# Performance work log

Measured on AMD Instinct MI355X. Metric: run time of the kernel, lower is better.

Reference implementation:

```python
import jax, jax.numpy as jnp
import numpy as np

LN_EPS = 1e-5

def _moe_forward(x, Wg, bg, W1, b1, W2, b2, ln_w, ln_b, gate_scale, top_k=2):
    B, N, D = x.shape
    E = Wg.shape[1]
    x_flat = x.reshape(B * N, D)                      # [T, D]
    # --- router (MoEGate): softmax -> top-k -> renormalize ---
    logits = x_flat @ Wg + bg                         # [T, E]
    probs = jax.nn.softmax(logits, axis=-1)
    w, idx = jax.lax.top_k(probs, top_k)              # [T, k]
    w = w / jnp.sum(w, axis=-1, keepdims=True)
    # dense gate matrix [T, E]: scatter top-k weights onto their experts
    gates = jnp.sum(jax.nn.one_hot(idx, E, dtype=x.dtype) * w[..., None], axis=1)
    # --- experts: Linear -> GELU(erf) -> Linear, computed densely for all experts ---
    h = jax.nn.gelu(jnp.einsum('td,edo->eto', x_flat, W1) + b1[:, None, :],
                    approximate=False)                # [E, T, O]
    eo = jnp.einsum('eto,eoq->etq', h, W2) + b2[:, None, :]  # [E, T, O]
    # --- weighted combine (equivalent to masked scatter-add in the torch loop) ---
    out_flat = jnp.einsum('te,eto->to', gates, eo)    # [T, O]
    out = out_flat.reshape(B, N, -1) * gate_scale[0]
    # --- LayerNorm ---
    mu = jnp.mean(out, axis=-1, keepdims=True)
    var = jnp.var(out, axis=-1, keepdims=True)
    return (out - mu) / jnp.sqrt(var + LN_EPS) * ln_w + ln_b


def setup_inputs() -> dict:
    key = jax.random.key(0)
    ks = jax.random.split(key, 5)
    B, N, D, O, E = 8, 1024, 1024, 4096, 4
    return {
        'x': jax.random.normal(ks[0], (B, N, D), dtype=jnp.float32),
        'Wg': jax.random.normal(ks[1], (D, E), dtype=jnp.float32) * 0.02,
        'bg': jnp.zeros((E,), jnp.float32),
        'W1': jax.random.normal(ks[2], (E, D, O), dtype=jnp.float32) * (1.0 / np.sqrt(D)),
        'b1': jnp.zeros((E, O), jnp.float32),
        'W2': jax.random.normal(ks[3], (E, O, O), dtype=jnp.float32) * (1.0 / np.sqrt(O)),
        'b2': jnp.zeros((E, O), jnp.float32),
        'ln_w': jnp.ones((O,), jnp.float32),
        'ln_b': jnp.zeros((O,), jnp.float32),
        'gate_scale': jnp.ones((1,), jnp.float32) * 0.1,
    }


def reference(x, Wg, bg, W1, b1, W2, b2, ln_w, ln_b, gate_scale):
    return _moe_forward(x, Wg, bg, W1, b1, W2, b2, ln_w, ln_b, gate_scale)
```

## Files before the change

kernel.cpp:

```cpp
#include <hip/hip_runtime.h>
#include <cmath>


typedef float f32x4 __attribute__((ext_vector_type(4)));
typedef __bf16 bf16x8 __attribute__((ext_vector_type(8)));
typedef __bf16 bf16x4 __attribute__((ext_vector_type(4)));

#define T_TOK 8192
#define DDIM 1024
#define ODIM 4096
#define NEXP 4

__device__ __forceinline__ void gl_lds16(const void* g, void* l) {
    __builtin_amdgcn_global_load_lds(
        (const __attribute__((address_space(1))) void*)g,
        (__attribute__((address_space(3))) void*)l, 16, 0, 0);
}

__global__ __launch_bounds__(256) void cvt_bf16_vec(const float* __restrict__ in,
                                                    __bf16* __restrict__ out, int n4) {
    int i = blockIdx.x * 256 + threadIdx.x;
    if (i >= n4) return;
    float4 v = ((const float4*)in)[i];
    bf16x4 o = { (__bf16)v.x, (__bf16)v.y, (__bf16)v.z, (__bf16)v.w };
    ((bf16x4*)out)[i] = o;
}

__global__ __launch_bounds__(256) void transpose_cvt(const float* __restrict__ in,
                                                     __bf16* __restrict__ out,
                                                     int R, int C) {
    __shared__ float tile[32][33];
    const size_t eoff = (size_t)blockIdx.z * R * C;
    const float* ip = in + eoff;
    __bf16* op = out + eoff;
    const int c0 = blockIdx.x * 32, r0 = blockIdx.y * 32;
    const int tx = threadIdx.x, ty = threadIdx.y;
#pragma unroll
    for (int i = 0; i < 4; i++)
        tile[ty + i * 8][tx] = ip[(size_t)(r0 + ty + i * 8) * C + c0 + tx];
    __syncthreads();
#pragma unroll
    for (int i = 0; i < 4; i++)
        op[(size_t)(c0 + ty + i * 8) * R + r0 + tx] = (__bf16)tile[tx][ty + i * 8];
}

__global__ __launch_bounds__(256) void router_kernel(const float* __restrict__ x,
                                                     const float* __restrict__ Wg,
                                                     const float* __restrict__ bg,
                                                     int* __restrict__ counts,
                                                     int* __restrict__ perm,
                                                     float* __restrict__ wlist) {
    const int wave = threadIdx.x >> 6, lane = threadIdx.x & 63;
    const int t = blockIdx.x * 4 + wave;
    const float* xr = x + (size_t)t * DDIM;
    float a0 = 0.f, a1 = 0.f, a2 = 0.f, a3 = 0.f;
    const float4* Wg4 = (const float4*)Wg;
    for (int d = lane; d < DDIM; d += 64) {
        float xv = xr[d];
        float4 w = Wg4[d];
        a0 += xv * w.x; a1 += xv * w.y; a2 += xv * w.z; a3 += xv * w.w;
    }
#pragma unroll
    for (int off = 32; off; off >>= 1) {
        a0 += __shfl_xor(a0, off); a1 += __shfl_xor(a1, off);
        a2 += __shfl_xor(a2, off); a3 += __shfl_xor(a3, off);
    }
    if (lane == 0) {
        float l[4] = {a0 + bg[0], a1 + bg[1], a2 + bg[2], a3 + bg[3]};
        float mx = fmaxf(fmaxf(l[0], l[1]), fmaxf(l[2], l[3]));
        float p[4], s = 0.f;
#pragma unroll
        for (int e = 0; e < 4; e++) { p[e] = expf(l[e] - mx); s += p[e]; }
#pragma unroll
        for (int e = 0; e < 4; e++) p[e] /= s;
        int e1 = 0;
#pragma unroll
        for (int e = 1; e < 4; e++) if (p[e] > p[e1]) e1 = e;
        int e2 = (e1 == 0) ? 1 : 0;
#pragma unroll
        for (int e = 0; e < 4; e++) if (e != e1 && p[e] > p[e2]) e2 = e;
        const float inv = 1.0f / (p[e1] + p[e2]);
        int pos1 = atomicAdd(&counts[e1], 1);
        perm[e1 * T_TOK + pos1] = t;
        wlist[e1 * T_TOK + pos1] = p[e1] * inv;
        int pos2 = atomicAdd(&counts[e2], 1);
        perm[e2 * T_TOK + pos2] = t;
        wlist[e2 * T_TOK + pos2] = p[e2] * inv;
    }
}

template <int MODE, int KDIM>
__global__ __launch_bounds__(256) void moe_gemm(const __bf16* __restrict__ A,
                                                const __bf16* __restrict__ B,
                                                const float* __restrict__ bias,
                                                __bf16* __restrict__ Hout,
                                                float* __restrict__ Fout,
                                                const int* __restrict__ perm,
                                                const float* __restrict__ wlist,
                                                const int* __restrict__ countp) {
    constexpr int BK = 32;
    __shared__ __align__(16) __bf16 As[128 * BK];
    __shared__ __align__(16) __bf16 Bs[128 * BK];
    const int count = *countp;
    const int m0 = blockIdx.y * 128;
    if (m0 >= count) return;
    const int tid = threadIdx.x;
    const int wave = tid >> 6, lane = tid & 63;
    const int r16 = lane & 15, quad = lane >> 4;
    const int n0 = blockIdx.x * 128;
    const int wm = (wave & 1) * 64, wn = (wave >> 1) * 64;

    const int c0 = tid, c1 = tid + 256;
    const __bf16 *Ag0, *Ag1;
    if (MODE == 0) {
        Ag0 = A + (size_t)perm[m0 + (c0 >> 2)] * KDIM + (c0 & 3) * 8;
        Ag1 = A + (size_t)perm[m0 + (c1 >> 2)] * KDIM + (c1 & 3) * 8;
    } else {
        Ag0 = A + (size_t)(m0 + (c0 >> 2)) * KDIM + (c0 & 3) * 8;
        Ag1 = A + (size_t)(m0 + (c1 >> 2)) * KDIM + (c1 & 3) * 8;
    }
    const __bf16* Bg0 = B + (size_t)(n0 + (c0 >> 2)) * KDIM + (c0 & 3) * 8;
    const __bf16* Bg1 = B + (size_t)(n0 + (c1 >> 2)) * KDIM + (c1 & 3) * 8;
    __bf16* sA0 = &As[(wave * 64) * 8];
    __bf16* sA1 = &As[(256 + wave * 64) * 8];
    __bf16* sB0 = &Bs[(wave * 64) * 8];
    __bf16* sB1 = &Bs[(256 + wave * 64) * 8];

    f32x4 acc[4][4] = {};

    for (int k0 = 0; k0 < KDIM; k0 += BK) {
        gl_lds16(Ag0 + k0, sA0);
        gl_lds16(Ag1 + k0, sA1);
        gl_lds16(Bg0 + k0, sB0);
        gl_lds16(Bg1 + k0, sB1);
        __syncthreads();
        bf16x8 af[4], bfr[4];
#pragma unroll
        for (int i = 0; i < 4; i++)
            af[i] = *(const bf16x8*)&As[(wm + i * 16 + r16) * BK + quad * 8];
#pragma unroll
        for (int i = 0; i < 4; i++)
            bfr[i] = *(const bf16x8*)&Bs[(wn + i * 16 + r16) * BK + quad * 8];
#pragma unroll
        for (int mi = 0; mi < 4; mi++)
#pragma unroll
            for (int ni = 0; ni < 4; ni++)
                acc[mi][ni] = __builtin_amdgcn_mfma_f32_16x16x32_bf16(
                    af[mi], bfr[ni], acc[mi][ni], 0, 0, 0);
        __syncthreads();
    }

    const int colBase = n0 + wn + r16;
    if (MODE == 0) {
#pragma unroll
        for (int mi = 0; mi < 4; mi++) {
            const int rowBase = m0 + wm + mi * 16 + quad * 4;
#pragma unroll
            for (int ni = 0; ni < 4; ni++) {
                const int col = colBase + ni * 16;
                const float bv = bias[col];
#pragma unroll
                for (int r = 0; r < 4; r++) {
                    if (rowBase + r < count) {
                        float xv = acc[mi][ni][r] + bv;
                        float u = 1.5957691216057308f * xv * (1.0f + 0.044715f * xv * xv);
                        float gv = xv * __builtin_amdgcn_rcpf(1.0f + __expf(-u));
                        Hout[(size_t)(rowBase + r) * ODIM + col] = (__bf16)gv;
                    }
                }
            }
        }
    } else {
#pragma unroll
        for (int mi = 0; mi < 4; mi++) {
            const int rowBase = m0 + wm + mi * 16 + quad * 4;
            int tok[4]; float g[4]; bool ok[4];
#pragma unroll
            for (int r = 0; r < 4; r++) {
                const int i = rowBase + r;
                ok[r] = (i < count);
                tok[r] = ok[r] ? perm[i] : 0;
                g[r] = ok[r] ? wlist[i] : 0.f;
            }
#pragma unroll
            for (int ni = 0; ni < 4; ni++) {
                const int col = colBase + ni * 16;
                const float bv = bias[col];
#pragma unroll
                for (int r = 0; r < 4; r++) {
                    if (ok[r]) {
                        float v = g[r] * (acc[mi][ni][r] + bv);
                        Fout[(size_t)tok[r] * ODIM + col] += v;
                    }
                }
            }
        }
    }
}

__global__ __launch_bounds__(256) void ln_kernel(float* __restrict__ out,
                                                 const float* __restrict__ lw,
                                                 const float* __restrict__ lb,
                                                 const float* __restrict__ gsp) {
    const int t = blockIdx.x;
    float* row = out + (size_t)t * ODIM;
    const float gs = gsp[0];
    float4 v[4];
    float s = 0.f, ss = 0.f;
#pragma unroll
    for (int i = 0; i < 4; i++) {
        float4 a = ((const float4*)row)[threadIdx.x + i * 256];
        a.x *= gs; a.y *= gs; a.z *= gs; a.w *= gs;
        v[i] = a;
        s += a.x + a.y + a.z + a.w;
        ss += a.x * a.x + a.y * a.y + a.z * a.z + a.w * a.w;
    }
#pragma unroll
    for (int off = 32; off; off >>= 1) {
        s += __shfl_xor(s, off);
        ss += __shfl_xor(ss, off);
    }
    __shared__ float rs[4], rss[4];
    const int wave = threadIdx.x >> 6, lane = threadIdx.x & 63;
    if (lane == 0) { rs[wave] = s; rss[wave] = ss; }
    __syncthreads();
    s = rs[0] + rs[1] + rs[2] + rs[3];
    ss = rss[0] + rss[1] + rss[2] + rss[3];
    const float mu = s * (1.0f / ODIM);
    const float var = ss * (1.0f / ODIM) - mu * mu;
    const float inv = 1.0f / sqrtf(var + 1e-5f);
#pragma unroll
    for (int i = 0; i < 4; i++) {
        const int c4 = threadIdx.x + i * 256;
        float4 w4 = ((const float4*)lw)[c4];
        float4 b4 = ((const float4*)lb)[c4];
        float4 o;
        o.x = (v[i].x - mu) * inv * w4.x + b4.x;
        o.y = (v[i].y - mu) * inv * w4.y + b4.y;
        o.z = (v[i].z - mu) * inv * w4.z + b4.z;
        o.w = (v[i].w - mu) * inv * w4.w + b4.w;
        ((float4*)row)[c4] = o;
    }
}

extern "C" void kernel_launch(void* const* d_in, const int* in_sizes, int n_in,
                              void* d_out, int out_size, void* d_ws, size_t ws_size,
                              hipStream_t stream) {
    const float* x   = (const float*)d_in[0];
    const float* Wg  = (const float*)d_in[1];
    const float* bg  = (const float*)d_in[2];
    const float* W1  = (const float*)d_in[3];
    const float* b1  = (const float*)d_in[4];
    const float* W2  = (const float*)d_in[5];
    const float* b2  = (const float*)d_in[6];
    const float* lnw = (const float*)d_in[7];
    const float* lnb = (const float*)d_in[8];
    const float* gsc = (const float*)d_in[9];
    float* out = (float*)d_out;

    char* w = (char*)d_ws;
    __bf16* Xb  = (__bf16*)w;
    __bf16* W1T = Xb + (size_t)T_TOK * DDIM;
    __bf16* W2T = W1T + (size_t)NEXP * ODIM * DDIM;
    __bf16* H   = W2T + (size_t)NEXP * ODIM * ODIM;
    int*   counts = (int*)(H + (size_t)T_TOK * ODIM);
    int*   perm   = counts + NEXP;
    float* wlist  = (float*)(perm + NEXP * T_TOK);

    hipMemsetAsync(counts, 0, (NEXP + 2 * NEXP * T_TOK) * sizeof(int) , stream);
    hipMemsetAsync(out, 0, (size_t)T_TOK * ODIM * sizeof(float), stream);

    cvt_bf16_vec<<<(T_TOK * DDIM / 4) / 256, 256, 0, stream>>>(x, Xb, T_TOK * DDIM / 4);
    dim3 tb(32, 8);
    transpose_cvt<<<dim3(ODIM / 32, DDIM / 32, NEXP), tb, 0, stream>>>(W1, W1T, DDIM, ODIM);
    transpose_cvt<<<dim3(ODIM / 32, ODIM / 32, NEXP), tb, 0, stream>>>(W2, W2T, ODIM, ODIM);
    router_kernel<<<T_TOK / 4, 256, 0, stream>>>(x, Wg, bg, counts, perm, wlist);

    for (int e = 0; e < NEXP; e++) {
        moe_gemm<0, DDIM><<<dim3(ODIM / 128, T_TOK / 128), 256, 0, stream>>>(
            Xb, W1T + (size_t)e * ODIM * DDIM, b1 + e * ODIM,
            H, nullptr, perm + e * T_TOK, nullptr, counts + e);
        moe_gemm<1, ODIM><<<dim3(ODIM / 128, T_TOK / 128), 256, 0, stream>>>(
            H, W2T + (size_t)e * ODIM * ODIM, b2 + e * ODIM,
            nullptr, out, perm + e * T_TOK, wlist + e * T_TOK, counts + e);
    }
    ln_kernel<<<T_TOK, 256, 0, stream>>>(out, lnw, lnb, gsc);
}
```

Baseline: 2.045 ms.

## Double GEMM K-tile with XOR-swizzled LDS, vectorize transpose, atomic combine

The MoE GEMM now uses a K tile of 64 instead of 32, halving the barrier pairs per K loop. It adds an XOR swizzle on the LDS column chunks to avoid bank conflicts on the wider rows. The weight transpose-convert kernel switches to 64x64 tiles with float4 loads and bf16x4 stores to cut memory transactions. The second GEMM's read-modify-write accumulation becomes unsafeAtomicAdd, which removes a load and may change float summation order.

```diff
diff --git a/kernel.cpp b/kernel.cpp
--- a/kernel.cpp
+++ b/kernel.cpp
@@ -29,19 +29,29 @@
 __global__ __launch_bounds__(256) void transpose_cvt(const float* __restrict__ in,
                                                      __bf16* __restrict__ out,
                                                      int R, int C) {
-    __shared__ float tile[32][33];
+    __shared__ float tile[64][65];
     const size_t eoff = (size_t)blockIdx.z * R * C;
     const float* ip = in + eoff;
     __bf16* op = out + eoff;
-    const int c0 = blockIdx.x * 32, r0 = blockIdx.y * 32;
-    const int tx = threadIdx.x, ty = threadIdx.y;
-#pragma unroll
-    for (int i = 0; i < 4; i++)
-        tile[ty + i * 8][tx] = ip[(size_t)(r0 + ty + i * 8) * C + c0 + tx];
+    const int c0 = blockIdx.x * 64, r0 = blockIdx.y * 64;
+    const int tid = threadIdx.x;
+    const int rr = tid >> 4, c4 = (tid & 15) * 4;
+#pragma unroll
+    for (int i = 0; i < 4; i++) {
+        const int r = rr + i * 16;
+        float4 v = *(const float4*)(ip + (size_t)(r0 + r) * C + c0 + c4);
+        tile[r][c4 + 0] = v.x; tile[r][c4 + 1] = v.y;
+        tile[r][c4 + 2] = v.z; tile[r][c4 + 3] = v.w;
+    }
     __syncthreads();
-#pragma unroll
-    for (int i = 0; i < 4; i++)
-        op[(size_t)(c0 + ty + i * 8) * R + r0 + tx] = (__bf16)tile[tx][ty + i * 8];
+    const int cc = tid >> 4, r4 = (tid & 15) * 4;
+#pragma unroll
+    for (int i = 0; i < 4; i++) {
+        const int c = cc + i * 16;
+        bf16x4 o = { (__bf16)tile[r4 + 0][c], (__bf16)tile[r4 + 1][c],
+                     (__bf16)tile[r4 + 2][c], (__bf16)tile[r4 + 3][c] };
+        *(bf16x4*)(op + (size_t)(c0 + c) * R + r0 + r4) = o;
+    }
 }
 
 __global__ __launch_bounds__(256) void router_kernel(const float* __restrict__ x,
@@ -98,7 +108,7 @@
                                                 const int* __restrict__ perm,
                                                 const float* __restrict__ wlist,
                                                 const int* __restrict__ countp) {
-    constexpr int BK = 32;
+    constexpr int BK = 64;
     __shared__ __align__(16) __bf16 As[128 * BK];
     __shared__ __align__(16) __bf16 Bs[128 * BK];
     const int count = *countp;
@@ -110,43 +120,52 @@
     const int n0 = blockIdx.x * 128;
     const int wm = (wave & 1) * 64, wn = (wave >> 1) * 64;
 
-    const int c0 = tid, c1 = tid + 256;
-    const __bf16 *Ag0, *Ag1;
-    if (MODE == 0) {
-        Ag0 = A + (size_t)perm[m0 + (c0 >> 2)] * KDIM + (c0 & 3) * 8;
-        Ag1 = A + (size_t)perm[m0 + (c1 >> 2)] * KDIM + (c1 & 3) * 8;
-    } else {
-        Ag0 = A + (size_t)(m0 + (c0 >> 2)) * KDIM + (c0 & 3) * 8;
-        Ag1 = A + (size_t)(m0 + (c1 >> 2)) * KDIM + (c1 & 3) * 8;
-    }
-    const __bf16* Bg0 = B + (size_t)(n0 + (c0 >> 2)) * KDIM + (c0 & 3) * 8;
-    const __bf16* Bg1 = B + (size_t)(n0 + (c1 >> 2)) * KDIM + (c1 & 3) * 8;
-    __bf16* sA0 = &As[(wave * 64) * 8];
-    __bf16* sA1 = &As[(256 + wave * 64) * 8];
-    __bf16* sB0 = &Bs[(wave * 64) * 8];
-    __bf16* sB1 = &Bs[(256 + wave * 64) * 8];
+    const __bf16 *Ag[4], *Bg[4];
+    __bf16 *sA[4], *sB[4];
+#pragma unroll
+    for (int g = 0; g < 4; g++) {
+        const int c = tid + g * 256;
+        const int row = c >> 3;
+        const int col = (((c & 7) ^ (row & 7))) * 8;
+        if (MODE == 0)
+            Ag[g] = A + (size_t)perm[m0 + row] * KDIM + col;
+        else
+            Ag[g] = A + (size_t)(m0 + row) * KDIM + col;
+        Bg[g] = B + (size_t)(n0 + row) * KDIM + col;
+        sA[g] = &As[(g * 256 + wave * 64) * 8];
+        sB[g] = &Bs[(g * 256 + wave * 64) * 8];
+    }
 
     f32x4 acc[4][4] = {};
 
     for (int k0 = 0; k0 < KDIM; k0 += BK) {
-        gl_lds16(Ag0 + k0, sA0);
-        gl_lds16(Ag1 + k0, sA1);
-        gl_lds16(Bg0 + k0, sB0);
-        gl_lds16(Bg1 + k0, sB1);
+#pragma unroll
+        for (int g = 0; g < 4; g++) gl_lds16(Ag[g] + k0, sA[g]);
+#pragma unroll
+        for (int g = 0; g < 4; g++) gl_lds16(Bg[g] + k0, sB[g]);
         __syncthreads();
-        bf16x8 af[4], bfr[4];
-#pragma unroll
-        for (int i = 0; i < 4; i++)
-            af[i] = *(const bf16x8*)&As[(wm + i * 16 + r16) * BK + quad * 8];
-#pragma unroll
-        for (int i = 0; i < 4; i++)
-            bfr[i] = *(const bf16x8*)&Bs[(wn + i * 16 + r16) * BK + quad * 8];
-#pragma unroll
-        for (int mi = 0; mi < 4; mi++)
-#pragma unroll
-            for (int ni = 0; ni < 4; ni++)
-                acc[mi][ni] = __builtin_amdgcn_mfma_f32_16x16x32_bf16(
-                    af[mi], bfr[ni], acc[mi][ni], 0, 0, 0);
+#pragma unroll
+        for (int kk = 0; kk < 2; kk++) {
+            bf16x8 af[4], bfr[4];
+#pragma unroll
+            for (int i = 0; i < 4; i++) {
+                const int row = wm + i * 16 + r16;
+                const int cc = (kk * 4 + quad) ^ (row & 7);
+                af[i] = *(const bf16x8*)&As[row * BK + cc * 8];
+            }
+#pragma unroll
+            for (int i = 0; i < 4; i++) {
+                const int row = wn + i * 16 + r16;
+                const int cc = (kk * 4 + quad) ^ (row & 7);
+                bfr[i] = *(const bf16x8*)&Bs[row * BK + cc * 8];
+            }
+#pragma unroll
+            for (int mi = 0; mi < 4; mi++)
+#pragma unroll
+                for (int ni = 0; ni < 4; ni++)
+                    acc[mi][ni] = __builtin_amdgcn_mfma_f32_16x16x32_bf16(
+                        af[mi], bfr[ni], acc[mi][ni], 0, 0, 0);
+        }
         __syncthreads();
     }
 
@@ -189,8 +208,8 @@
 #pragma unroll
                 for (int r = 0; r < 4; r++) {
                     if (ok[r]) {
-                        float v = g[r] * (acc[mi][ni][r] + bv);
-                        Fout[(size_t)tok[r] * ODIM + col] += v;
+                        unsafeAtomicAdd(&Fout[(size_t)tok[r] * ODIM + col],
+                                        g[r] * (acc[mi][ni][r] + bv));
                     }
                 }
             }
@@ -267,13 +286,12 @@
     int*   perm   = counts + NEXP;
     float* wlist  = (float*)(perm + NEXP * T_TOK);
 
-    hipMemsetAsync(counts, 0, (NEXP + 2 * NEXP * T_TOK) * sizeof(int) , stream);
+    hipMemsetAsync(counts, 0, (NEXP + 2 * NEXP * T_TOK) * sizeof(int), stream);
     hipMemsetAsync(out, 0, (size_t)T_TOK * ODIM * sizeof(float), stream);
 
     cvt_bf16_vec<<<(T_TOK * DDIM / 4) / 256, 256, 0, stream>>>(x, Xb, T_TOK * DDIM / 4);
-    dim3 tb(32, 8);
-    transpose_cvt<<<dim3(ODIM / 32, DDIM / 32, NEXP), tb, 0, stream>>>(W1, W1T, DDIM, ODIM);
-    transpose_cvt<<<dim3(ODIM / 32, ODIM / 32, NEXP), tb, 0, stream>>>(W2, W2T, ODIM, ODIM);
+    transpose_cvt<<<dim3(ODIM / 64, DDIM / 64, NEXP), 256, 0, stream>>>(W1, W1T, DDIM, ODIM);
+    transpose_cvt<<<dim3(ODIM / 64, ODIM / 64, NEXP), 256, 0, stream>>>(W2, W2T, ODIM, ODIM);
     router_kernel<<<T_TOK / 4, 256, 0, stream>>>(x, Wg, bg, counts, perm, wlist);
 
     for (int e = 0; e < NEXP; e++) {
```

After: 2.200 ms. 7.6% more time.
